# Performance work log

Hardware: AMD Instinct MI355X
Metric: run time of the kernel (lower is better)

The kernel has to match this reference:

```python
import jax, jax.numpy as jnp
import numpy as np

N = 50000   # nodes
E = 1600000 # edges
D = 64      # feature dim


def gcn_conv(x, edge_index, W, b):
    """PyG GCNConv: x' = D^-1/2 (A+I) D^-1/2 (x W) + b."""
    n = x.shape[0]
    xw = x @ W                                   # [N, D_out] linear first (PyG order)
    loop = jnp.arange(n)
    src = jnp.concatenate([edge_index[0], loop])  # add self-loops
    dst = jnp.concatenate([edge_index[1], loop])
    deg = jax.ops.segment_sum(jnp.ones_like(src, dtype=xw.dtype), dst, num_segments=n)
    dinv = jnp.where(deg > 0, jax.lax.rsqrt(deg), 0.0)
    norm = dinv[src] * dinv[dst]                  # symmetric normalization
    out = jax.ops.segment_sum(norm[:, None] * xw[src], dst, num_segments=n)
    return out + b


def setup_inputs() -> dict:
    key = jax.random.key(0)
    k1, k2, k3, k4 = jax.random.split(key, 4)
    x = jax.random.normal(k1, (N, D), dtype=jnp.float32)
    edge_index = jax.random.randint(k2, (2, E), 0, N, dtype=jnp.int64)
    s = 1.0 / np.sqrt(D)
    W1 = jax.random.normal(k3, (D, D), dtype=jnp.float32) * s
    b1 = jnp.zeros((D,), dtype=jnp.float32)
    W2 = jax.random.normal(k4, (D, D), dtype=jnp.float32) * s
    b2 = jnp.zeros((D,), dtype=jnp.float32)
    return {"x": x, "edge_index": edge_index, "W1": W1, "b1": b1, "W2": W2, "b2": b2}


def reference(x, edge_index, W1, b1, W2, b2):
    h = gcn_conv(x, edge_index, W1, b1)
    h = jax.nn.relu(h)  # dropout is identity in eval mode
    out = gcn_conv(h, edge_index, W2, b2)
    return out
```

## Files before the change

kernel.cpp:

```cpp
#include <hip/hip_runtime.h>
#include <hip/hip_fp16.h>


#define P1_EDGES 4096
#define BSTRIDE 32768

__global__ void bucket_kernel(const int* __restrict__ src, const int* __restrict__ dst,
                              unsigned* __restrict__ cursor, unsigned* __restrict__ ebuf,
                              int e, int B) {
    __shared__ unsigned hist[128];
    __shared__ unsigned base[128];
    for (int i = threadIdx.x; i < B; i += 1024) hist[i] = 0;
    __syncthreads();
    int e0 = blockIdx.x * P1_EDGES;
    unsigned bk[4], rk[4], pk[4];
    bool vk[4];
#pragma unroll
    for (int k = 0; k < 4; ++k) {
        int t = e0 + k * 1024 + threadIdx.x;
        vk[k] = (t < e);
        bk[k] = 0; rk[k] = 0; pk[k] = 0;
        if (vk[k]) {
            unsigned s = (unsigned)src[t], d = (unsigned)dst[t];
            unsigned b = d >> 9;
            bk[k] = b;
            rk[k] = atomicAdd(&hist[b], 1u);
            pk[k] = (d << 16) | s;
        }
    }
    __syncthreads();
    for (int i = threadIdx.x; i < B; i += 1024)
        base[i] = hist[i] ? atomicAdd(&cursor[i], hist[i]) : 0u;
    __syncthreads();
#pragma unroll
    for (int k = 0; k < 4; ++k)
        if (vk[k]) {
            unsigned slot = base[bk[k]] + rk[k];
            if (slot < (unsigned)BSTRIDE)
                ebuf[(size_t)bk[k] * BSTRIDE + slot] = pk[k];
        }
}

__global__ void scan_buckets(const unsigned* __restrict__ bcnt, unsigned* __restrict__ bstart,
                             unsigned* __restrict__ rpf, int B, int n, int e) {
    __shared__ unsigned sh[128];
    unsigned v = (threadIdx.x < (unsigned)B) ? bcnt[threadIdx.x] : 0u;
    sh[threadIdx.x] = v;
    __syncthreads();
    for (int off = 1; off < 128; off <<= 1) {
        unsigned t = (threadIdx.x >= (unsigned)off) ? sh[threadIdx.x - off] : 0u;
        __syncthreads();
        sh[threadIdx.x] += t;
        __syncthreads();
    }
    if (threadIdx.x < (unsigned)B) bstart[threadIdx.x] = sh[threadIdx.x] - v;
    if (threadIdx.x == 0) { bstart[B] = (unsigned)e; rpf[n] = (unsigned)e; }
}

__global__ void statsfill_kernel(const unsigned* __restrict__ ebuf,
                                 const unsigned* __restrict__ bcnt,
                                 const unsigned* __restrict__ bstart,
                                 unsigned* __restrict__ rpf, float* __restrict__ dinv,
                                 unsigned short* __restrict__ csr, int n) {
    __shared__ unsigned pos[512];
    __shared__ unsigned sh[512];
    __shared__ unsigned rpl[512];
    int b = blockIdx.x;
    int w0 = b << 9;
    int wlen = min(w0 + 512, n) - w0;
    if (threadIdx.x < 512) pos[threadIdx.x] = 0;
    __syncthreads();
    unsigned cnt = bcnt[b];
    const unsigned* eb = ebuf + (size_t)b * BSTRIDE;
    for (unsigned j = threadIdx.x; j < cnt; j += 1024)
        atomicAdd(&pos[(eb[j] >> 16) - w0], 1u);
    __syncthreads();
    unsigned v = 0;
    if (threadIdx.x < 512) { v = pos[threadIdx.x]; sh[threadIdx.x] = v; }
    __syncthreads();
    for (int off = 1; off < 512; off <<= 1) {
        unsigned t = 0;
        if (threadIdx.x < 512 && threadIdx.x >= (unsigned)off) t = sh[threadIdx.x - off];
        __syncthreads();
        if (threadIdx.x < 512) sh[threadIdx.x] += t;
        __syncthreads();
    }
    if (threadIdx.x < 512) {
        unsigned rp = bstart[b] + sh[threadIdx.x] - v;
        rpl[threadIdx.x] = rp;
        if ((int)threadIdx.x < wlen) {
            rpf[w0 + threadIdx.x] = rp;
            dinv[w0 + threadIdx.x] = rsqrtf((float)v + 1.0f);
        }
        pos[threadIdx.x] = 0;
    }
    __syncthreads();
    for (unsigned j = threadIdx.x; j < cnt; j += 1024) {
        unsigned p = eb[j];
        unsigned d = (p >> 16) - w0;
        unsigned r = atomicAdd(&pos[d], 1u);
        csr[rpl[d] + r] = (unsigned short)(p & 0xffffu);
    }
}

__global__ void gemm64_kernel(const float4* __restrict__ X4, const float* __restrict__ W,
                              const float* __restrict__ dinv, __half* __restrict__ Yh, int n) {
    __shared__ float4 Ws[64][16];
    for (int i = threadIdx.x; i < 64 * 16; i += blockDim.x)
        Ws[i >> 4][i & 15] = ((const float4*)W)[i];
    __syncthreads();
    int lane = threadIdx.x & 63;
    int l = lane & 15;
    int gbase = lane & 48;
    int wid = blockIdx.x * (blockDim.x >> 6) + (threadIdx.x >> 6);
    int row = wid * 4 + (lane >> 4);
    if (row >= n) return;
    float4 xv = X4[(size_t)row * 16 + l];
    float4 acc = make_float4(0.f, 0.f, 0.f, 0.f);
#pragma unroll
    for (int k = 0; k < 64; ++k) {
        float comp = (k & 3) == 0 ? xv.x : (k & 3) == 1 ? xv.y : (k & 3) == 2 ? xv.z : xv.w;
        float a = __shfl(comp, gbase + (k >> 2));
        float4 w = Ws[k][l];
        acc.x = fmaf(a, w.x, acc.x); acc.y = fmaf(a, w.y, acc.y);
        acc.z = fmaf(a, w.z, acc.z); acc.w = fmaf(a, w.w, acc.w);
    }
    float di = dinv[row];
    __half2 h0 = __floats2half2_rn(acc.x * di, acc.y * di);
    __half2 h1 = __floats2half2_rn(acc.z * di, acc.w * di);
    uint2 o;
    o.x = *(const unsigned*)&h0;
    o.y = *(const unsigned*)&h1;
    *(uint2*)(Yh + (size_t)row * 64 + 4 * l) = o;
}

struct f8 { float4 a, b; };

__device__ __forceinline__ f8 aggregate_row8(const __half* __restrict__ xwh,
                                             const unsigned* __restrict__ csrw,
                                             unsigned start, unsigned end,
                                             int row, int l8, int gbase) {
    f8 acc;
    {
        uint4 hv = *(const uint4*)(xwh + (size_t)row * 64 + 8 * l8);
        float2 f0 = __half22float2(*(const __half2*)&hv.x);
        float2 f1 = __half22float2(*(const __half2*)&hv.y);
        float2 f2 = __half22float2(*(const __half2*)&hv.z);
        float2 f3 = __half22float2(*(const __half2*)&hv.w);
        acc.a = make_float4(f0.x, f0.y, f1.x, f1.y);
        acc.b = make_float4(f2.x, f2.y, f3.x, f3.y);
    }
    unsigned wb = start >> 1;
    unsigned jw = wb + (unsigned)l8;
    unsigned ed = (jw * 2 < end) ? __builtin_nontemporal_load(&csrw[jw]) : 0u;
    for (unsigned base = wb; base * 2 < end; base += 8) {
        unsigned jn = base + 8 + (unsigned)l8;
        unsigned ed_next = (jn * 2 < end) ? __builtin_nontemporal_load(&csrw[jn]) : 0u;
#pragma unroll
        for (int t = 0; t < 8; ++t) {
            unsigned p = __shfl(ed, gbase + t);
            unsigned i0 = (base + (unsigned)t) * 2;
            int s0 = (int)(p & 0xffffu);
            int s1 = (int)(p >> 16);
            float w0 = (i0 >= start && i0 < end) ? 1.0f : 0.0f;
            float w1 = (i0 + 1 < end) ? 1.0f : 0.0f;
            uint4 hv0 = *(const uint4*)(xwh + (size_t)s0 * 64 + 8 * l8);
            uint4 hv1 = *(const uint4*)(xwh + (size_t)s1 * 64 + 8 * l8);
            float2 a0 = __half22float2(*(const __half2*)&hv0.x);
            float2 a1 = __half22float2(*(const __half2*)&hv0.y);
            float2 a2 = __half22float2(*(const __half2*)&hv0.z);
            float2 a3 = __half22float2(*(const __half2*)&hv0.w);
            acc.a.x = fmaf(w0, a0.x, acc.a.x); acc.a.y = fmaf(w0, a0.y, acc.a.y);
            acc.a.z = fmaf(w0, a1.x, acc.a.z); acc.a.w = fmaf(w0, a1.y, acc.a.w);
            acc.b.x = fmaf(w0, a2.x, acc.b.x); acc.b.y = fmaf(w0, a2.y, acc.b.y);
            acc.b.z = fmaf(w0, a3.x, acc.b.z); acc.b.w = fmaf(w0, a3.y, acc.b.w);
            float2 c0 = __half22float2(*(const __half2*)&hv1.x);
            float2 c1 = __half22float2(*(const __half2*)&hv1.y);
            float2 c2 = __half22float2(*(const __half2*)&hv1.z);
            float2 c3 = __half22float2(*(const __half2*)&hv1.w);
            acc.a.x = fmaf(w1, c0.x, acc.a.x); acc.a.y = fmaf(w1, c0.y, acc.a.y);
            acc.a.z = fmaf(w1, c1.x, acc.a.z); acc.a.w = fmaf(w1, c1.y, acc.a.w);
            acc.b.x = fmaf(w1, c2.x, acc.b.x); acc.b.y = fmaf(w1, c2.y, acc.b.y);
            acc.b.z = fmaf(w1, c3.x, acc.b.z); acc.b.w = fmaf(w1, c3.y, acc.b.w);
        }
        ed = ed_next;
    }
    return acc;
}

__global__ void gather_gemm_kernel(const __half* __restrict__ xwh, const unsigned* __restrict__ csrw,
                                   const unsigned* __restrict__ row_ptr, const float* __restrict__ dinv,
                                   const float* __restrict__ b1, const float* __restrict__ W2,
                                   __half* __restrict__ Yh, int n) {
    __shared__ float4 Ws[64][16];
    for (int i = threadIdx.x; i < 64 * 16; i += blockDim.x)
        Ws[i >> 4][i & 15] = ((const float4*)W2)[i];
    __syncthreads();
    int lane = threadIdx.x & 63;
    int l8 = lane & 7;
    int gbase = lane & 56;
    int wid = blockIdx.x * (blockDim.x >> 6) + (threadIdx.x >> 6);
    int row = wid * 8 + (lane >> 3);
    if (row >= n) return;
    float di = dinv[row];
    f8 acc = aggregate_row8(xwh, csrw, row_ptr[row], row_ptr[row + 1], row, l8, gbase);
    float4 ba = ((const float4*)b1)[2 * l8];
    float4 bb = ((const float4*)b1)[2 * l8 + 1];
    float h0 = fmaxf(fmaf(di, acc.a.x, ba.x), 0.f);
    float h1 = fmaxf(fmaf(di, acc.a.y, ba.y), 0.f);
    float h2 = fmaxf(fmaf(di, acc.a.z, ba.z), 0.f);
    float h3 = fmaxf(fmaf(di, acc.a.w, ba.w), 0.f);
    float h4 = fmaxf(fmaf(di, acc.b.x, bb.x), 0.f);
    float h5 = fmaxf(fmaf(di, acc.b.y, bb.y), 0.f);
    float h6 = fmaxf(fmaf(di, acc.b.z, bb.z), 0.f);
    float h7 = fmaxf(fmaf(di, acc.b.w, bb.w), 0.f);
    float4 o0 = make_float4(0.f, 0.f, 0.f, 0.f);
    float4 o1 = make_float4(0.f, 0.f, 0.f, 0.f);
#pragma unroll
    for (int k = 0; k < 64; ++k) {
        float comp = (k & 7) == 0 ? h0 : (k & 7) == 1 ? h1 : (k & 7) == 2 ? h2 :
                     (k & 7) == 3 ? h3 : (k & 7) == 4 ? h4 : (k & 7) == 5 ? h5 :
                     (k & 7) == 6 ? h6 : h7;
        float a = __shfl(comp, gbase + (k >> 3));
        float4 w0 = Ws[k][2 * l8];
        float4 w1 = Ws[k][2 * l8 + 1];
        o0.x = fmaf(a, w0.x, o0.x); o0.y = fmaf(a, w0.y, o0.y);
        o0.z = fmaf(a, w0.z, o0.z); o0.w = fmaf(a, w0.w, o0.w);
        o1.x = fmaf(a, w1.x, o1.x); o1.y = fmaf(a, w1.y, o1.y);
        o1.z = fmaf(a, w1.z, o1.z); o1.w = fmaf(a, w1.w, o1.w);
    }
    __half2 p0 = __floats2half2_rn(o0.x * di, o0.y * di);
    __half2 p1 = __floats2half2_rn(o0.z * di, o0.w * di);
    __half2 p2 = __floats2half2_rn(o1.x * di, o1.y * di);
    __half2 p3 = __floats2half2_rn(o1.z * di, o1.w * di);
    uint4 o;
    o.x = *(const unsigned*)&p0; o.y = *(const unsigned*)&p1;
    o.z = *(const unsigned*)&p2; o.w = *(const unsigned*)&p3;
    *(uint4*)(Yh + (size_t)row * 64 + 8 * l8) = o;
}

__global__ void gather_out_kernel(const __half* __restrict__ xwh, const unsigned* __restrict__ csrw,
                                  const unsigned* __restrict__ row_ptr, const float* __restrict__ dinv,
                                  const float* __restrict__ bias, float4* __restrict__ out4, int n) {
    int lane = threadIdx.x & 63;
    int l8 = lane & 7;
    int gbase = lane & 56;
    int wid = blockIdx.x * (blockDim.x >> 6) + (threadIdx.x >> 6);
    int row = wid * 8 + (lane >> 3);
    if (row >= n) return;
    float di = dinv[row];
    f8 acc = aggregate_row8(xwh, csrw, row_ptr[row], row_ptr[row + 1], row, l8, gbase);
    float4 ba = ((const float4*)bias)[2 * l8];
    float4 bb = ((const float4*)bias)[2 * l8 + 1];
    float4 oa, ob;
    oa.x = fmaf(di, acc.a.x, ba.x); oa.y = fmaf(di, acc.a.y, ba.y);
    oa.z = fmaf(di, acc.a.z, ba.z); oa.w = fmaf(di, acc.a.w, ba.w);
    ob.x = fmaf(di, acc.b.x, bb.x); ob.y = fmaf(di, acc.b.y, bb.y);
    ob.z = fmaf(di, acc.b.z, bb.z); ob.w = fmaf(di, acc.b.w, bb.w);
    out4[(size_t)row * 16 + 2 * l8]     = oa;
    out4[(size_t)row * 16 + 2 * l8 + 1] = ob;
}

extern "C" void kernel_launch(void* const* d_in, const int* in_sizes, int n_in,
                              void* d_out, int out_size, void* d_ws, size_t ws_size,
                              hipStream_t stream) {
    const float* x  = (const float*)d_in[0];
    const int*   ei = (const int*)d_in[1];
    const float* W1 = (const float*)d_in[2];
    const float* b1 = (const float*)d_in[3];
    const float* W2 = (const float*)d_in[4];
    const float* b2 = (const float*)d_in[5];
    const int n = in_sizes[0] / 64;
    const int e = in_sizes[1] / 2;
    const int* src = ei;
    const int* dst = ei + e;

    char* ws = (char*)d_ws;
    size_t off = 0;
    auto alloc = [&](size_t bytes) -> void* {
        void* p = ws + off;
        off = (off + bytes + 255) & ~(size_t)255;
        return p;
    };
    unsigned* rpf    = (unsigned*)alloc((size_t)(n + 1) * 4);
    float*    dinv   = (float*)alloc((size_t)n * 4);
    unsigned* bstart = (unsigned*)alloc(129 * 4);
    unsigned* cursor = (unsigned*)alloc(128 * 4);
    unsigned short* csr = (unsigned short*)alloc(((size_t)e / 2 + 64) * 4);
    const int B = (n + 511) / 512;
    size_t ebuf_sz = (size_t)B * BSTRIDE * 4;
    size_t ov = ebuf_sz > (size_t)n * 64 * 2 ? ebuf_sz : (size_t)n * 64 * 2;
    char*     overlay = (char*)alloc(ov);
    unsigned* ebuf    = (unsigned*)overlay;
    __half*   xwh1    = (__half*)overlay;
    __half*   xwh2    = (__half*)alloc((size_t)n * 64 * 2);
    float*    outf    = (float*)d_out;

    const int nbP1 = (e + P1_EDGES - 1) / P1_EDGES;

    hipMemsetAsync(cursor, 0, 128 * 4, stream);
    bucket_kernel<<<nbP1, 1024, 0, stream>>>(src, dst, cursor, ebuf, e, B);
    scan_buckets<<<1, 128, 0, stream>>>(cursor, bstart, rpf, B, n, e);
    statsfill_kernel<<<B, 1024, 0, stream>>>(ebuf, cursor, bstart, rpf, dinv, csr, n);

    const int gblk16 = (n + 15) / 16;
    const int gblk32 = (n + 31) / 32;

    gemm64_kernel<<<gblk16, 256, 0, stream>>>((const float4*)x, W1, dinv, xwh1, n);
    gather_gemm_kernel<<<gblk32, 256, 0, stream>>>(xwh1, (const unsigned*)csr, rpf, dinv, b1, W2, xwh2, n);

    gather_out_kernel<<<gblk32, 256, 0, stream>>>(xwh2, (const unsigned*)csr, rpf, dinv, b2, (float4*)outf, n);
}
```

Measured before the change: 180.8 us.

## Halve bucket width, fuse bucket scan via last-block, vectorize edge loads

Buckets now cover 256 destination nodes instead of 512, doubling the number of statsfill blocks so more CUs are busy. The separate scan kernel is removed: the last bucket block, detected with a done counter, performs the prefix scan, which saves a launch. Edge indices are read as int4 and the final output uses nontemporal stores. The smaller per-bucket stride risks overflow on skewed degree distributions.

Measured after the change: 399.2 us. 2.21x slower.

```diff
diff --git a/kernel.cpp b/kernel.cpp
--- a/kernel.cpp
+++ b/kernel.cpp
@@ -3,26 +3,41 @@
 
 
 #define P1_EDGES 4096
-#define BSTRIDE 32768
+#define BSTRIDE 16384
+
+typedef float vfloat4 __attribute__((ext_vector_type(4)));
 
 __global__ void bucket_kernel(const int* __restrict__ src, const int* __restrict__ dst,
-                              unsigned* __restrict__ cursor, unsigned* __restrict__ ebuf,
-                              int e, int B) {
-    __shared__ unsigned hist[128];
-    __shared__ unsigned base[128];
+                              unsigned* __restrict__ cursor, unsigned* __restrict__ done,
+                              unsigned* __restrict__ ebuf, unsigned* __restrict__ bstart,
+                              unsigned* __restrict__ rpf, int e, int B, int n) {
+    __shared__ unsigned hist[256];
+    __shared__ unsigned base[256];
+    __shared__ unsigned amlast;
     for (int i = threadIdx.x; i < B; i += 1024) hist[i] = 0;
     __syncthreads();
     int e0 = blockIdx.x * P1_EDGES;
+    int tbase = e0 + (int)threadIdx.x * 4;
+    int4 sv = make_int4(0, 0, 0, 0), dv = make_int4(0, 0, 0, 0);
+    if (tbase + 3 < e) {
+        sv = ((const int4*)(src + e0))[threadIdx.x];
+        dv = ((const int4*)(dst + e0))[threadIdx.x];
+    } else {
+        if (tbase + 0 < e) { sv.x = src[tbase + 0]; dv.x = dst[tbase + 0]; }
+        if (tbase + 1 < e) { sv.y = src[tbase + 1]; dv.y = dst[tbase + 1]; }
+        if (tbase + 2 < e) { sv.z = src[tbase + 2]; dv.z = dst[tbase + 2]; }
+    }
     unsigned bk[4], rk[4], pk[4];
     bool vk[4];
 #pragma unroll
     for (int k = 0; k < 4; ++k) {
-        int t = e0 + k * 1024 + threadIdx.x;
+        int t = tbase + k;
         vk[k] = (t < e);
         bk[k] = 0; rk[k] = 0; pk[k] = 0;
         if (vk[k]) {
-            unsigned s = (unsigned)src[t], d = (unsigned)dst[t];
-            unsigned b = d >> 9;
+            unsigned s = (unsigned)(k == 0 ? sv.x : k == 1 ? sv.y : k == 2 ? sv.z : sv.w);
+            unsigned d = (unsigned)(k == 0 ? dv.x : k == 1 ? dv.y : k == 2 ? dv.z : dv.w);
+            unsigned b = d >> 8;
             bk[k] = b;
             rk[k] = atomicAdd(&hist[b], 1u);
             pk[k] = (d << 16) | s;
@@ -39,21 +54,23 @@
             if (slot < (unsigned)BSTRIDE)
                 ebuf[(size_t)bk[k] * BSTRIDE + slot] = pk[k];
         }
-}
-
-__global__ void scan_buckets(const unsigned* __restrict__ bcnt, unsigned* __restrict__ bstart,
-                             unsigned* __restrict__ rpf, int B, int n, int e) {
-    __shared__ unsigned sh[128];
-    unsigned v = (threadIdx.x < (unsigned)B) ? bcnt[threadIdx.x] : 0u;
-    sh[threadIdx.x] = v;
-    __syncthreads();
-    for (int off = 1; off < 128; off <<= 1) {
-        unsigned t = (threadIdx.x >= (unsigned)off) ? sh[threadIdx.x - off] : 0u;
+    __threadfence();
+    if (threadIdx.x == 0)
+        amlast = (atomicAdd(done, 1u) == (unsigned)gridDim.x - 1u) ? 1u : 0u;
+    __syncthreads();
+    if (!amlast) return;
+    unsigned v = 0;
+    if (threadIdx.x < (unsigned)B) v = atomicAdd(&cursor[threadIdx.x], 0u);
+    if (threadIdx.x < 256) hist[threadIdx.x] = v;
+    __syncthreads();
+    for (int off = 1; off < 256; off <<= 1) {
+        unsigned t = 0;
+        if (threadIdx.x < 256 && threadIdx.x >= (unsigned)off) t = hist[threadIdx.x - off];
         __syncthreads();
-        sh[threadIdx.x] += t;
+        if (threadIdx.x < 256) hist[threadIdx.x] += t;
         __syncthreads();
     }
-    if (threadIdx.x < (unsigned)B) bstart[threadIdx.x] = sh[threadIdx.x] - v;
+    if (threadIdx.x < (unsigned)B) bstart[threadIdx.x] = hist[threadIdx.x] - v;
     if (threadIdx.x == 0) { bstart[B] = (unsigned)e; rpf[n] = (unsigned)e; }
 }
 
@@ -62,13 +79,13 @@
                                  const unsigned* __restrict__ bstart,
                                  unsigned* __restrict__ rpf, float* __restrict__ dinv,
                                  unsigned short* __restrict__ csr, int n) {
-    __shared__ unsigned pos[512];
-    __shared__ unsigned sh[512];
-    __shared__ unsigned rpl[512];
+    __shared__ unsigned pos[256];
+    __shared__ unsigned sh[256];
+    __shared__ unsigned rpl[256];
     int b = blockIdx.x;
-    int w0 = b << 9;
-    int wlen = min(w0 + 512, n) - w0;
-    if (threadIdx.x < 512) pos[threadIdx.x] = 0;
+    int w0 = b << 8;
+    int wlen = min(w0 + 256, n) - w0;
+    if (threadIdx.x < 256) pos[threadIdx.x] = 0;
     __syncthreads();
     unsigned cnt = bcnt[b];
     const unsigned* eb = ebuf + (size_t)b * BSTRIDE;
@@ -76,16 +93,16 @@
         atomicAdd(&pos[(eb[j] >> 16) - w0], 1u);
     __syncthreads();
     unsigned v = 0;
-    if (threadIdx.x < 512) { v = pos[threadIdx.x]; sh[threadIdx.x] = v; }
-    __syncthreads();
-    for (int off = 1; off < 512; off <<= 1) {
+    if (threadIdx.x < 256) { v = pos[threadIdx.x]; sh[threadIdx.x] = v; }
+    __syncthreads();
+    for (int off = 1; off < 256; off <<= 1) {
         unsigned t = 0;
-        if (threadIdx.x < 512 && threadIdx.x >= (unsigned)off) t = sh[threadIdx.x - off];
+        if (threadIdx.x < 256 && threadIdx.x >= (unsigned)off) t = sh[threadIdx.x - off];
         __syncthreads();
-        if (threadIdx.x < 512) sh[threadIdx.x] += t;
+        if (threadIdx.x < 256) sh[threadIdx.x] += t;
         __syncthreads();
     }
-    if (threadIdx.x < 512) {
+    if (threadIdx.x < 256) {
         unsigned rp = bstart[b] + sh[threadIdx.x] - v;
         rpl[threadIdx.x] = rp;
         if ((int)threadIdx.x < wlen) {
@@ -252,13 +269,14 @@
     f8 acc = aggregate_row8(xwh, csrw, row_ptr[row], row_ptr[row + 1], row, l8, gbase);
     float4 ba = ((const float4*)bias)[2 * l8];
     float4 bb = ((const float4*)bias)[2 * l8 + 1];
-    float4 oa, ob;
+    vfloat4 oa, ob;
     oa.x = fmaf(di, acc.a.x, ba.x); oa.y = fmaf(di, acc.a.y, ba.y);
     oa.z = fmaf(di, acc.a.z, ba.z); oa.w = fmaf(di, acc.a.w, ba.w);
     ob.x = fmaf(di, acc.b.x, bb.x); ob.y = fmaf(di, acc.b.y, bb.y);
     ob.z = fmaf(di, acc.b.z, bb.z); ob.w = fmaf(di, acc.b.w, bb.w);
-    out4[(size_t)row * 16 + 2 * l8]     = oa;
-    out4[(size_t)row * 16 + 2 * l8 + 1] = ob;
+    vfloat4* o4 = (vfloat4*)out4;
+    __builtin_nontemporal_store(oa, &o4[(size_t)row * 16 + 2 * l8]);
+    __builtin_nontemporal_store(ob, &o4[(size_t)row * 16 + 2 * l8 + 1]);
 }
 
 extern "C" void kernel_launch(void* const* d_in, const int* in_sizes, int n_in,
@@ -284,10 +302,11 @@
     };
     unsigned* rpf    = (unsigned*)alloc((size_t)(n + 1) * 4);
     float*    dinv   = (float*)alloc((size_t)n * 4);
-    unsigned* bstart = (unsigned*)alloc(129 * 4);
-    unsigned* cursor = (unsigned*)alloc(128 * 4);
+    unsigned* bstart = (unsigned*)alloc(256 * 4);
+    unsigned* cursor = (unsigned*)alloc(257 * 4);
+    unsigned* done   = cursor + 256;
     unsigned short* csr = (unsigned short*)alloc(((size_t)e / 2 + 64) * 4);
-    const int B = (n + 511) / 512;
+    const int B = (n + 255) / 256;
     size_t ebuf_sz = (size_t)B * BSTRIDE * 4;
     size_t ov = ebuf_sz > (size_t)n * 64 * 2 ? ebuf_sz : (size_t)n * 64 * 2;
     char*     overlay = (char*)alloc(ov);
@@ -298,9 +317,8 @@
 
     const int nbP1 = (e + P1_EDGES - 1) / P1_EDGES;
 
-    hipMemsetAsync(cursor, 0, 128 * 4, stream);
-    bucket_kernel<<<nbP1, 1024, 0, stream>>>(src, dst, cursor, ebuf, e, B);
-    scan_buckets<<<1, 128, 0, stream>>>(cursor, bstart, rpf, B, n, e);
+    hipMemsetAsync(cursor, 0, 257 * 4, stream);
+    bucket_kernel<<<nbP1, 1024, 0, stream>>>(src, dst, cursor, done, ebuf, bstart, rpf, e, B, n);
     statsfill_kernel<<<B, 1024, 0, stream>>>(ebuf, cursor, bstart, rpf, dinv, csr, n);
 
     const int gblk16 = (n + 15) / 16;
```
